# Kernel optimization log

Measured on AMD Instinct MI355X. Metric: run time of the kernel, lower is better.

## Reference

```python
import jax, jax.numpy as jnp
import numpy as np

B, C_IN, C_OUT, H, K = 64, 64, 128, 1855, 6


def setup_inputs() -> dict:
    key = jax.random.key(0)
    k1, k2, k3, k4 = jax.random.split(key, 4)
    x = jax.random.normal(k1, (B, C_IN, H), dtype=jnp.float32)
    # neighbor table [H, K]; valid indices first, -1 padding at the end
    neighbors = jax.random.randint(k2, (H, K), 0, H)
    n_boundary = H // 10
    neighbors = neighbors.at[:n_boundary, K - 2:].set(-1)
    weight_center = jax.random.normal(k3, (C_OUT, C_IN), dtype=jnp.float32) / np.sqrt(C_IN).astype(np.float32)
    weight_neighbors = jax.random.normal(k4, (C_OUT, C_IN, K), dtype=jnp.float32) / np.sqrt(C_IN * K).astype(np.float32)
    bias = jnp.zeros((C_OUT,), dtype=jnp.float32)
    return {
        "x": x,
        "neighbors": neighbors,
        "weight_center": weight_center,
        "weight_neighbors": weight_neighbors,
        "bias": bias,
    }


def reference(x, neighbors, weight_center, weight_neighbors, bias):
    # x: [B, C_in, H]; neighbors: [H, K] with -1 = invalid (valid-first ordering)
    mask = neighbors >= 0                               # [H, K]
    idx = jnp.where(mask, neighbors, 0)                 # safe gather indices
    gathered = x[:, :, idx] * mask.astype(x.dtype)[None, None, :, :]  # [B, C_in, H, K]
    center = jnp.einsum('bch,oc->boh', x, weight_center)              # [B, C_out, H]
    neigh = jnp.einsum('bchk,ock->boh', gathered, weight_neighbors)   # [B, C_out, H]
    counts = (1 + mask.sum(axis=-1)).astype(x.dtype)                  # [H]
    return (center + neigh) / counts[None, None, :] + bias[None, :, None]
```

## Files before the change

### kernel.cpp

```cpp
#include <hip/hip_runtime.h>
#include <stdint.h>

typedef __bf16 bf16x8 __attribute__((ext_vector_type(8)));
typedef float floatx4 __attribute__((ext_vector_type(4)));
typedef unsigned int u32x4 __attribute__((ext_vector_type(4)));
typedef unsigned short u16;
typedef unsigned short u16x8 __attribute__((ext_vector_type(8)));
typedef unsigned int u32;

#define CIN   64
#define COUT  128
#define H_    1855
#define KNB   6
#define KTOT  448
#define NSTEPS 14

#define HLROW 2064
#define BUFSZ 33024

#define WP_OFF     ((size_t)H_ * 4096 * 2)
#define CINV_OFF   (WP_OFF + (size_t)COUT * KTOT * 2)
#define ZERO_OFF   (CINV_OFF + 7424)
#define SRCOFF_OFF (ZERO_OFF + 1024)
#define INVOFF 0xFFFFFFFFu

#define PIN4(v) asm volatile("" : "+v"(v))

typedef __attribute__((address_space(1))) unsigned int as1_u32;
typedef __attribute__((address_space(3))) unsigned int as3_u32;
static __device__ __forceinline__ void ld16_to_lds(const void* g, void* l) {
    __builtin_amdgcn_global_load_lds((const as1_u32*)g, (as3_u32*)l, 16, 0, 0);
}

static __device__ inline u16 f32_to_bf16(float f) {
    u32 u = __float_as_uint(f);
    u32 r = (u + 0x7FFFu + ((u >> 16) & 1u)) >> 16;
    return (u16)r;
}

__global__ __launch_bounds__(256) void k_transpose(const float* __restrict__ x,
                                                   u16* __restrict__ xt3) {
    __shared__ u16 tile[64][65];
    int h0  = blockIdx.x * 64;
    int bc0 = blockIdx.y * 64;
    int tid  = threadIdx.x;
    int lane = tid & 63;
    int rowq = tid >> 6;
    int h = h0 + lane;
    bool hv = h < H_;
#pragma unroll
    for (int i = 0; i < 16; ++i) {
        int row = i * 4 + rowq;
        u16 v = 0;
        if (hv) v = f32_to_bf16(x[(size_t)(bc0 + row) * H_ + h]);
        tile[row][lane] = v;
    }
    __syncthreads();
    int bg = tid & 7;
    int hb = tid >> 3;
#pragma unroll
    for (int ii = 0; ii < 2; ++ii) {
        int hl = ii * 32 + hb;
        int hh = h0 + hl;
        u16x8 v;
#pragma unroll
        for (int j = 0; j < 8; ++j) v[j] = tile[bg * 8 + j][hl];
        if (hh < H_)
            *(u16x8*)(xt3 + (size_t)hh * 4096 + bc0 + bg * 8) = v;
    }
}

__global__ __launch_bounds__(256) void k_pack(const float* __restrict__ wc,
                                              const float* __restrict__ wn,
                                              const int* __restrict__ nbr,
                                              u16* __restrict__ wp,
                                              float* __restrict__ cInvG,
                                              u32* __restrict__ zeroPg,
                                              u32* __restrict__ srcOff) {
    int tg = blockIdx.x * 256 + threadIdx.x;
    if (tg < 64) zeroPg[tg] = 0u;
    if (tg < H_) {
        int cnt = 1;
#pragma unroll
        for (int j = 0; j < KNB; ++j) cnt += (nbr[tg * KNB + j] >= 0) ? 1 : 0;
        cInvG[tg] = 1.0f / (float)cnt;
    }
    if (tg < H_ * 8) {
        int h = tg >> 3, s = tg & 7;
        u32 e;
        if (s == 0) e = (u32)h * 8192u;
        else if (s <= 6) {
            int n = nbr[h * KNB + (s - 1)];
            e = (n >= 0) ? (u32)n * 8192u : INVOFF;
        } else e = INVOFF;
        srcOff[tg] = e;
    }
    if (tg >= COUT * KTOT) return;
    int o = tg / KTOT;
    int rem = tg - o * KTOT;
    int s = rem >> 6, c = rem & 63;
    float v = (s == 0) ? wc[o * CIN + c]
                       : wn[(o * CIN + c) * KNB + (s - 1)];
    wp[tg] = f32_to_bf16(v);
}

__global__ __launch_bounds__(256, 2) void k_main(const u16* __restrict__ xt3,
                                                 const u16* __restrict__ wp,
                                                 const float* __restrict__ bias,
                                                 const float* __restrict__ cInvG,
                                                 const u32* __restrict__ srcOff,
                                                 float* __restrict__ out) {
    __shared__ __align__(16) char LDS[2 * BUFSZ];

    int tid  = threadIdx.x;
    int gbl  = blockIdx.x;
    int bp   = gbl & 31;
    int hs   = gbl >> 5;
    int b0   = bp * 2;
    int h0   = hs * 64;

    int lane = tid & 63;
    int wave = tid >> 6;
    int col  = lane & 15;
    int quad = lane >> 4;
    int m0w  = wave * 32;
    int lane16 = lane & 15;
    int ssub = lane >> 4;
    int bl   = lane16 >> 3;
    int chunk = lane16 & 7;

    const char* xb = (const char*)xt3;

    u32x4 afrag[2][NSTEPS];
#pragma unroll
    for (int mt = 0; mt < 2; ++mt) {
        int o = m0w + mt * 16 + col;
#pragma unroll
        for (int kk = 0; kk < NSTEPS; ++kk)
            afrag[mt][kk] = *(const u32x4*)(wp + o * KTOT + kk * 32 + quad * 8);
    }
#pragma unroll
    for (int mt = 0; mt < 2; ++mt)
#pragma unroll
        for (int kk = 0; kk < NSTEPS; ++kk)
            PIN4(afrag[mt][kk]);

    float biasv[2][4];
#pragma unroll
    for (int mt = 0; mt < 2; ++mt)
#pragma unroll
        for (int r = 0; r < 4; ++r)
            biasv[mt][r] = bias[m0w + mt * 16 + quad * 4 + r];

    float icv[4];
#pragma unroll
    for (int t = 0; t < 4; ++t) {
        int hic = h0 + t * 16 + col;
        icv[t] = cInvG[hic < H_ ? hic : 0];
    }

    u32 colOff = (u32)((b0 + bl) * 128 + chunk * 16);
    u32 zOff   = (u32)ZERO_OFF + (u32)(lane16 * 16);
    u32 offs[4][8];
#pragma unroll
    for (int t = 0; t < 4; ++t)
#pragma unroll
        for (int i = 0; i < 8; ++i) {
            int hh = h0 + t * 16 + wave * 4 + (i & 3);
            int s  = (i >> 2) * 4 + ssub;
            u32 e = (hh < H_) ? srcOff[hh * 8 + s] : INVOFF;
            offs[t][i] = (e == INVOFF) ? zOff : (e + colOff);
        }

    int rb0 = col * HLROW + quad * 16;
    int rb1 = rb0 + 128;
    char* buf0 = LDS;
    char* buf1 = LDS + BUFSZ;
    float* E = (float*)(LDS + BUFSZ);

#define STAGE(t, bufp) do {                                                   \
    char* _d = (bufp) + (wave * 4) * HLROW;                                   \
    _Pragma("unroll")                                                         \
    for (int _i = 0; _i < 8; ++_i)                                            \
        ld16_to_lds(xb + offs[t][_i], _d + (_i & 3) * HLROW + (_i >> 2) * 1024); \
} while (0)

#define COMPUTE(accv, bufp) do {                                              \
    _Pragma("unroll") for (int _m = 0; _m < 2; ++_m)                          \
    _Pragma("unroll") for (int _n = 0; _n < 2; ++_n)                          \
        accv[_m][_n] = (floatx4){0.0f, 0.0f, 0.0f, 0.0f};                     \
    __builtin_amdgcn_s_setprio(1);                                            \
    _Pragma("unroll")                                                         \
    for (int kk = 0; kk < NSTEPS; ++kk) {                                     \
        int koff = (kk >> 1) * 256 + (kk & 1) * 64;                           \
        bf16x8 bfa = *(const bf16x8*)((bufp) + rb0 + koff);                   \
        bf16x8 bfb = *(const bf16x8*)((bufp) + rb1 + koff);                   \
        bf16x8 a0 = __builtin_bit_cast(bf16x8, afrag[0][kk]);                 \
        bf16x8 a1 = __builtin_bit_cast(bf16x8, afrag[1][kk]);                 \
        accv[0][0] = __builtin_amdgcn_mfma_f32_16x16x32_bf16(a0, bfa, accv[0][0], 0, 0, 0); \
        accv[1][0] = __builtin_amdgcn_mfma_f32_16x16x32_bf16(a1, bfa, accv[1][0], 0, 0, 0); \
        accv[0][1] = __builtin_amdgcn_mfma_f32_16x16x32_bf16(a0, bfb, accv[0][1], 0, 0, 0); \
        accv[1][1] = __builtin_amdgcn_mfma_f32_16x16x32_bf16(a1, bfb, accv[1][1], 0, 0, 0); \
    }                                                                         \
    __builtin_amdgcn_s_setprio(0);                                            \
} while (0)

#define EPIW(pp, t, accv) do {                                                \
    float _ic = icv[(pp) * 2 + (t)];                                          \
    _Pragma("unroll") for (int _m = 0; _m < 2; ++_m)                          \
    _Pragma("unroll") for (int _n = 0; _n < 2; ++_n)                          \
    _Pragma("unroll") for (int _r = 0; _r < 4; ++_r) {                        \
        int _row = m0w + _m * 16 + quad * 4 + _r;                             \
        int _idx = ((_n) * 32 + (t) * 16 + col) ^ (quad << 3);                \
        E[_row * 64 + _idx] = accv[_m][_n][_r] * _ic + biasv[_m][_r];         \
    }                                                                         \
} while (0)

#define EPIS(pp) do {                                                         \
    int _h5 = lane & 31, _g = lane >> 5;                                      \
    int _hh = h0 + (pp) * 32 + _h5;                                           \
    bool _hv = _hh < H_;                                                      \
    size_t _ob = (size_t)(b0 + _g) * ((size_t)COUT * H_)                      \
               + (size_t)m0w * H_ + _hh;                                      \
    _Pragma("unroll")                                                         \
    for (int _j = 0; _j < 32; ++_j) {                                         \
        float _v = E[(m0w + _j) * 64 + ((_g * 32 + _h5) ^ (((_j >> 2) & 3) << 3))]; \
        if (_hv) out[_ob + (size_t)_j * H_] = _v;                             \
    }                                                                         \
} while (0)

#define ABAR0()  do { asm volatile("s_waitcnt vmcnt(0) lgkmcnt(0)" ::: "memory");  __builtin_amdgcn_s_barrier(); } while (0)
#define ABAR32() do { asm volatile("s_waitcnt vmcnt(32) lgkmcnt(0)" ::: "memory"); __builtin_amdgcn_s_barrier(); } while (0)
#define BBAR()   do { asm volatile("s_waitcnt lgkmcnt(0)" ::: "memory");           __builtin_amdgcn_s_barrier(); } while (0)

    floatx4 accA[2][2], accB[2][2];

    STAGE(0, buf0);
    ABAR0();
    STAGE(1, buf1);
    COMPUTE(accA, buf0);
    ABAR0();
    STAGE(2, buf0);
    COMPUTE(accB, buf1);
    BBAR();
    EPIW(0, 0, accA);
    EPIW(0, 1, accB);
    EPIS(0);
    ABAR32();
    STAGE(3, buf1);
    COMPUTE(accA, buf0);
    ABAR0();
    COMPUTE(accB, buf1);
    BBAR();
    EPIW(1, 0, accA);
    EPIW(1, 1, accB);
    EPIS(1);

#undef STAGE
#undef COMPUTE
#undef EPIW
#undef EPIS
#undef ABAR0
#undef ABAR32
#undef BBAR
}

extern "C" void kernel_launch(void* const* d_in, const int* in_sizes, int n_in,
                              void* d_out, int out_size, void* d_ws, size_t ws_size,
                              hipStream_t stream) {
    const float* x    = (const float*)d_in[0];
    const int*   nbr  = (const int*)d_in[1];
    const float* wc   = (const float*)d_in[2];
    const float* wn   = (const float*)d_in[3];
    const float* bias = (const float*)d_in[4];

    u16*   xt3    = (u16*)d_ws;
    u16*   wp     = (u16*)((char*)d_ws + WP_OFF);
    float* cInvG  = (float*)((char*)d_ws + CINV_OFF);
    u32*   zeroPg = (u32*)((char*)d_ws + ZERO_OFF);
    u32*   srcOff = (u32*)((char*)d_ws + SRCOFF_OFF);

    k_pack<<<dim3((COUT * KTOT + 255) / 256), dim3(256), 0, stream>>>(
        wc, wn, nbr, wp, cInvG, zeroPg, srcOff);
    k_transpose<<<dim3(29, 64), dim3(256), 0, stream>>>(x, xt3);
    k_main<<<dim3(928), dim3(256), 0, stream>>>(
        xt3, wp, bias, cInvG, srcOff, (float*)d_out);
}
```

Measured before the change: 134.5 us.

## Merge prep kernels, vectorize transpose loads, and split main kernel over eight waves

Folds the weight/neighbor packing kernel into the transpose kernel as an extra grid row, which removes one launch. The transpose's global reads become 4-wide float loads. The main kernel now runs 512 threads with eight waves, each owning 16 output channels instead of 32, which halves per-wave A-fragment registers and staging loads. The epilogue staging moves to per-wave regions of the LDS buffers with adjusted waitcnts. The aim is more waves per CU and better latency hiding, at the cost of more barrier participants and less A-fragment reuse per wave.

Measured after the change: 210.0 us. 1.56x slower.

```diff
diff --git a/kernel.cpp b/kernel.cpp
--- a/kernel.cpp
+++ b/kernel.cpp
@@ -3,6 +3,7 @@
 
 typedef __bf16 bf16x8 __attribute__((ext_vector_type(8)));
 typedef float floatx4 __attribute__((ext_vector_type(4)));
+typedef float floatx4u __attribute__((ext_vector_type(4), aligned(4)));
 typedef unsigned int u32x4 __attribute__((ext_vector_type(4)));
 typedef unsigned short u16;
 typedef unsigned short u16x8 __attribute__((ext_vector_type(8)));
@@ -16,6 +17,7 @@
 #define NSTEPS 14
 
 #define HLROW 2064
+#define WROW  4128
 #define BUFSZ 33024
 
 #define WP_OFF     ((size_t)H_ * 4096 * 2)
@@ -38,22 +40,68 @@
     return (u16)r;
 }
 
-__global__ __launch_bounds__(256) void k_transpose(const float* __restrict__ x,
-                                                   u16* __restrict__ xt3) {
+__global__ __launch_bounds__(256) void k_prep(const float* __restrict__ x,
+                                              const float* __restrict__ wc,
+                                              const float* __restrict__ wn,
+                                              const int* __restrict__ nbr,
+                                              u16* __restrict__ xt3,
+                                              u16* __restrict__ wp,
+                                              float* __restrict__ cInvG,
+                                              u32* __restrict__ zeroPg,
+                                              u32* __restrict__ srcOff) {
+    int tid = threadIdx.x;
+    if (blockIdx.y == 64) {
+        for (int tg = blockIdx.x * 256 + tid; tg < COUT * KTOT; tg += 29 * 256) {
+            if (tg < 64) zeroPg[tg] = 0u;
+            if (tg < H_) {
+                int cnt = 1;
+#pragma unroll
+                for (int j = 0; j < KNB; ++j) cnt += (nbr[tg * KNB + j] >= 0) ? 1 : 0;
+                cInvG[tg] = 1.0f / (float)cnt;
+            }
+            if (tg < H_ * 8) {
+                int h = tg >> 3, s = tg & 7;
+                u32 e;
+                if (s == 0) e = (u32)h * 8192u;
+                else if (s <= 6) {
+                    int n = nbr[h * KNB + (s - 1)];
+                    e = (n >= 0) ? (u32)n * 8192u : INVOFF;
+                } else e = INVOFF;
+                srcOff[tg] = e;
+            }
+            int o = tg / KTOT;
+            int rem = tg - o * KTOT;
+            int s = rem >> 6, c = rem & 63;
+            float v = (s == 0) ? wc[o * CIN + c]
+                               : wn[(o * CIN + c) * KNB + (s - 1)];
+            wp[tg] = f32_to_bf16(v);
+        }
+        return;
+    }
     __shared__ u16 tile[64][65];
     int h0  = blockIdx.x * 64;
     int bc0 = blockIdx.y * 64;
-    int tid  = threadIdx.x;
-    int lane = tid & 63;
-    int rowq = tid >> 6;
-    int h = h0 + lane;
-    bool hv = h < H_;
-#pragma unroll
-    for (int i = 0; i < 16; ++i) {
-        int row = i * 4 + rowq;
-        u16 v = 0;
-        if (hv) v = f32_to_bf16(x[(size_t)(bc0 + row) * H_ + h]);
-        tile[row][lane] = v;
+    int lh   = tid & 15;
+    int rowi = tid >> 4;
+    bool safe = (h0 + 64 <= H_);
+#pragma unroll
+    for (int i = 0; i < 4; ++i) {
+        int row = i * 16 + rowi;
+        int h = h0 + lh * 4;
+        u16 v4[4];
+        if (safe) {
+            floatx4u f = *(const floatx4u*)(x + (size_t)(bc0 + row) * H_ + h);
+#pragma unroll
+            for (int j = 0; j < 4; ++j) v4[j] = f32_to_bf16(f[j]);
+        } else {
+#pragma unroll
+            for (int j = 0; j < 4; ++j) {
+                int hh = h + j;
+                v4[j] = (hh < H_) ? f32_to_bf16(x[(size_t)(bc0 + row) * H_ + hh]) : (u16)0;
+            }
+        }
+#pragma unroll
+        for (int j = 0; j < 4; ++j) tile[row][lh * 4 + j] = v4[j];
     }
     __syncthreads();
     int bg = tid & 7;
@@ -70,41 +118,7 @@
     }
 }
 
-__global__ __launch_bounds__(256) void k_pack(const float* __restrict__ wc,
-                                              const float* __restrict__ wn,
-                                              const int* __restrict__ nbr,
-                                              u16* __restrict__ wp,
-                                              float* __restrict__ cInvG,
-                                              u32* __restrict__ zeroPg,
-                                              u32* __restrict__ srcOff) {
-    int tg = blockIdx.x * 256 + threadIdx.x;
-    if (tg < 64) zeroPg[tg] = 0u;
-    if (tg < H_) {
-        int cnt = 1;
-#pragma unroll
-        for (int j = 0; j < KNB; ++j) cnt += (nbr[tg * KNB + j] >= 0) ? 1 : 0;
-        cInvG[tg] = 1.0f / (float)cnt;
-    }
-    if (tg < H_ * 8) {
-        int h = tg >> 3, s = tg & 7;
-        u32 e;
-        if (s == 0) e = (u32)h * 8192u;
-        else if (s <= 6) {
-            int n = nbr[h * KNB + (s - 1)];
-            e = (n >= 0) ? (u32)n * 8192u : INVOFF;
-        } else e = INVOFF;
-        srcOff[tg] = e;
-    }
-    if (tg >= COUT * KTOT) return;
-    int o = tg / KTOT;
-    int rem = tg - o * KTOT;
-    int s = rem >> 6, c = rem & 63;
-    float v = (s == 0) ? wc[o * CIN + c]
-                       : wn[(o * CIN + c) * KNB + (s - 1)];
-    wp[tg] = f32_to_bf16(v);
-}
-
-__global__ __launch_bounds__(256, 2) void k_main(const u16* __restrict__ xt3,
+__global__ __launch_bounds__(512, 4) void k_main(const u16* __restrict__ xt3,
                                                  const u16* __restrict__ wp,
                                                  const float* __restrict__ bias,
                                                  const float* __restrict__ cInvG,
@@ -123,7 +137,7 @@
     int wave = tid >> 6;
     int col  = lane & 15;
     int quad = lane >> 4;
-    int m0w  = wave * 32;
+    int m0w  = wave * 16;
     int lane16 = lane & 15;
     int ssub = lane >> 4;
     int bl   = lane16 >> 3;
@@ -131,26 +145,19 @@
 
     const char* xb = (const char*)xt3;
 
-    u32x4 afrag[2][NSTEPS];
-#pragma unroll
-    for (int mt = 0; mt < 2; ++mt) {
-        int o = m0w + mt * 16 + col;
+    u32x4 afrag[NSTEPS];
+    {
+        int o = m0w + col;
 #pragma unroll
         for (int kk = 0; kk < NSTEPS; ++kk)
-            afrag[mt][kk] = *(const u32x4*)(wp + o * KTOT + kk * 32 + quad * 8);
-    }
-#pragma unroll
-    for (int mt = 0; mt < 2; ++mt)
-#pragma unroll
-        for (int kk = 0; kk < NSTEPS; ++kk)
-            PIN4(afrag[mt][kk]);
-
-    float biasv[2][4];
-#pragma unroll
-    for (int mt = 0; mt < 2; ++mt)
-#pragma unroll
-        for (int r = 0; r < 4; ++r)
-            biasv[mt][r] = bias[m0w + mt * 16 + quad * 4 + r];
+            afrag[kk] = *(const u32x4*)(wp + o * KTOT + kk * 32 + quad * 8);
+    }
+#pragma unroll
+    for (int kk = 0; kk < NSTEPS; ++kk) PIN4(afrag[kk]);
+
+    float biasv[4];
+#pragma unroll
+    for (int r = 0; r < 4; ++r) biasv[r] = bias[m0w + quad * 4 + r];
 
     float icv[4];
 #pragma unroll
@@ -161,13 +168,13 @@
 
     u32 colOff = (u32)((b0 + bl) * 128 + chunk * 16);
     u32 zOff   = (u32)ZERO_OFF + (u32)(lane16 * 16);
-    u32 offs[4][8];
+    u32 offs[4][4];
 #pragma unroll
     for (int t = 0; t < 4; ++t)
 #pragma unroll
-        for (int i = 0; i < 8; ++i) {
-            int hh = h0 + t * 16 + wave * 4 + (i & 3);
-            int s  = (i >> 2) * 4 + ssub;
+        for (int i = 0; i < 4; ++i) {
+            int hh = h0 + t * 16 + wave * 2 + (i & 1);
+            int s  = (i >> 1) * 4 + ssub;
             u32 e = (hh < H_) ? srcOff[hh * 8 + s] : INVOFF;
             offs[t][i] = (e == INVOFF) ? zOff : (e + colOff);
         }
@@ -176,64 +183,58 @@
     int rb1 = rb0 + 128;
     char* buf0 = LDS;
     char* buf1 = LDS + BUFSZ;
-    float* E = (float*)(LDS + BUFSZ);
 
 #define STAGE(t, bufp) do {                                                   \
-    char* _d = (bufp) + (wave * 4) * HLROW;                                   \
+    char* _d = (bufp) + wave * WROW;                                          \
     _Pragma("unroll")                                                         \
-    for (int _i = 0; _i < 8; ++_i)                                            \
-        ld16_to_lds(xb + offs[t][_i], _d + (_i & 3) * HLROW + (_i >> 2) * 1024); \
+    for (int _i = 0; _i < 4; ++_i)                                            \
+        ld16_to_lds(xb + offs[t][_i], _d + (_i & 1) * HLROW + (_i >> 1) * 1024); \
 } while (0)
 
 #define COMPUTE(accv, bufp) do {                                              \
-    _Pragma("unroll") for (int _m = 0; _m < 2; ++_m)                          \
-    _Pragma("unroll") for (int _n = 0; _n < 2; ++_n)                          \
-        accv[_m][_n] = (floatx4){0.0f, 0.0f, 0.0f, 0.0f};                     \
+    accv[0] = (floatx4){0.0f, 0.0f, 0.0f, 0.0f};                              \
+    accv[1] = (floatx4){0.0f, 0.0f, 0.0f, 0.0f};                              \
     __builtin_amdgcn_s_setprio(1);                                            \
     _Pragma("unroll")                                                         \
     for (int kk = 0; kk < NSTEPS; ++kk) {                                     \
         int koff = (kk >> 1) * 256 + (kk & 1) * 64;                           \
         bf16x8 bfa = *(const bf16x8*)((bufp) + rb0 + koff);                   \
         bf16x8 bfb = *(const bf16x8*)((bufp) + rb1 + koff);                   \
-        bf16x8 a0 = __builtin_bit_cast(bf16x8, afrag[0][kk]);                 \
-        bf16x8 a1 = __builtin_bit_cast(bf16x8, afrag[1][kk]);                 \
-        accv[0][0] = __builtin_amdgcn_mfma_f32_16x16x32_bf16(a0, bfa, accv[0][0], 0, 0, 0); \
-        accv[1][0] = __builtin_amdgcn_mfma_f32_16x16x32_bf16(a1, bfa, accv[1][0], 0, 0, 0); \
-        accv[0][1] = __builtin_amdgcn_mfma_f32_16x16x32_bf16(a0, bfb, accv[0][1], 0, 0, 0); \
-        accv[1][1] = __builtin_amdgcn_mfma_f32_16x16x32_bf16(a1, bfb, accv[1][1], 0, 0, 0); \
+        bf16x8 a = __builtin_bit_cast(bf16x8, afrag[kk]);                     \
+        accv[0] = __builtin_amdgcn_mfma_f32_16x16x32_bf16(a, bfa, accv[0], 0, 0, 0); \
+        accv[1] = __builtin_amdgcn_mfma_f32_16x16x32_bf16(a, bfb, accv[1], 0, 0, 0); \
     }                                                                         \
     __builtin_amdgcn_s_setprio(0);                                            \
 } while (0)
 
-#define EPIW(pp, t, accv) do {                                                \
+#define EPIW(Ew, pp, t, accv) do {                                            \
     float _ic = icv[(pp) * 2 + (t)];                                          \
-    _Pragma("unroll") for (int _m = 0; _m < 2; ++_m)                          \
     _Pragma("unroll") for (int _n = 0; _n < 2; ++_n)                          \
     _Pragma("unroll") for (int _r = 0; _r < 4; ++_r) {                        \
-        int _row = m0w + _m * 16 + quad * 4 + _r;                             \
         int _idx = ((_n) * 32 + (t) * 16 + col) ^ (quad << 3);                \
-        E[_row * 64 + _idx] = accv[_m][_n][_r] * _ic + biasv[_m][_r];         \
+        (Ew)[(quad * 4 + _r) * 64 + _idx] = accv[_n][_r] * _ic + biasv[_r];   \
     }                                                                         \
 } while (0)
 
-#define EPIS(pp) do {                                                         \
+#define EPIS(Ew, pp) do {                                                     \
     int _h5 = lane & 31, _g = lane >> 5;                                      \
     int _hh = h0 + (pp) * 32 + _h5;                                           \
     bool _hv = _hh < H_;                                                      \
     size_t _ob = (size_t)(b0 + _g) * ((size_t)COUT * H_)                      \
                + (size_t)m0w * H_ + _hh;                                      \
     _Pragma("unroll")                                                         \
-    for (int _j = 0; _j < 32; ++_j) {                                         \
-        float _v = E[(m0w + _j) * 64 + ((_g * 32 + _h5) ^ (((_j >> 2) & 3) << 3))]; \
+    for (int _j = 0; _j < 16; ++_j) {                                         \
+        float _v = (Ew)[_j * 64 + ((_g * 32 + _h5) ^ (((_j >> 2) & 3) << 3))]; \
         if (_hv) out[_ob + (size_t)_j * H_] = _v;                             \
     }                                                                         \
 } while (0)
 
 #define ABAR0()  do { asm volatile("s_waitcnt vmcnt(0) lgkmcnt(0)" ::: "memory");  __builtin_amdgcn_s_barrier(); } while (0)
-#define ABAR32() do { asm volatile("s_waitcnt vmcnt(32) lgkmcnt(0)" ::: "memory"); __builtin_amdgcn_s_barrier(); } while (0)
+#define ABAR20() do { asm volatile("s_waitcnt vmcnt(20) lgkmcnt(0)" ::: "memory"); __builtin_amdgcn_s_barrier(); } while (0)
 #define BBAR()   do { asm volatile("s_waitcnt lgkmcnt(0)" ::: "memory");           __builtin_amdgcn_s_barrier(); } while (0)
-
-    floatx4 accA[2][2], accB[2][2];
+#define LGW()    asm volatile("s_waitcnt lgkmcnt(0)" ::: "memory")
+
+    floatx4 accA[2], accB[2];
 
     STAGE(0, buf0);
     ABAR0();
@@ -243,26 +244,34 @@
     STAGE(2, buf0);
     COMPUTE(accB, buf1);
     BBAR();
-    EPIW(0, 0, accA);
-    EPIW(0, 1, accB);
-    EPIS(0);
-    ABAR32();
-    STAGE(3, buf1);
+    {
+        float* E1 = (float*)(buf1 + wave * WROW);
+        EPIW(E1, 0, 0, accA);
+        EPIW(E1, 0, 1, accB);
+        EPIS(E1, 0);
+        LGW();
+        STAGE(3, buf1);
+    }
+    ABAR20();
     COMPUTE(accA, buf0);
     ABAR0();
     COMPUTE(accB, buf1);
     BBAR();
-    EPIW(1, 0, accA);
-    EPIW(1, 1, accB);
-    EPIS(1);
+    {
+        float* E0 = (float*)(buf0 + wave * WROW);
+        EPIW(E0, 1, 0, accA);
+        EPIW(E0, 1, 1, accB);
+        EPIS(E0, 1);
+    }
 
 #undef STAGE
 #undef COMPUTE
 #undef EPIW
 #undef EPIS
 #undef ABAR0
-#undef ABAR32
+#undef ABAR20
 #undef BBAR
+#undef LGW
 }
 
 extern "C" void kernel_launch(void* const* d_in, const int* in_sizes, int n_in,
@@ -280,9 +289,8 @@
     u32*   zeroPg = (u32*)((char*)d_ws + ZERO_OFF);
     u32*   srcOff = (u32*)((char*)d_ws + SRCOFF_OFF);
 
-    k_pack<<<dim3((COUT * KTOT + 255) / 256), dim3(256), 0, stream>>>(
-        wc, wn, nbr, wp, cInvG, zeroPg, srcOff);
-    k_transpose<<<dim3(29, 64), dim3(256), 0, stream>>>(x, xt3);
-    k_main<<<dim3(928), dim3(256), 0, stream>>>(
+    k_prep<<<dim3(29, 65), dim3(256), 0, stream>>>(
+        x, wc, wn, nbr, xt3, wp, cInvG, zeroPg, srcOff);
+    k_main<<<dim3(928), dim3(512), 0, stream>>>(
         xt3, wp, bias, cInvG, srcOff, (float*)d_out);
 }
```
